# Performance work log

Measured on AMD Instinct MI355X. Metric: run time of the kernel, lower is better.

The kernel has to match this reference:

```python
import jax, jax.numpy as jnp
import numpy as np

B, T, D = 32, 2048, 128


def setup_inputs() -> dict:
    key = jax.random.key(0)
    k1, k2, k3 = jax.random.split(key, 3)
    values = jax.random.normal(k1, (B, T, D), dtype=jnp.float32)
    # monotonically increasing per-feature timestamps (irregular sampling)
    times = jnp.cumsum(jax.random.uniform(k2, (B, T, D), dtype=jnp.float32), axis=1)
    mask = jax.random.randint(k3, (B, T, D), 0, 2) > 0  # True = observed
    return {"values": values, "times": times, "mask": mask}


def _fill(x, t, mask):
    """Parallel forward fill (LOCF) and backward fill (NOCB) of x and t.

    Replaces the serial Keras RNN scan with cummax/cummin over observation
    indices followed by a gather. Matches ForwardCell semantics:
      forward : x init 0, t init times[:, 0, :]
      backward: x init 0, t init max(times, axis=1)
    """
    Tn = x.shape[1]
    ar = jnp.broadcast_to(jnp.arange(Tn, dtype=jnp.int32)[None, :, None], x.shape)
    # ---- forward fill ----
    fidx = jax.lax.cummax(jnp.where(mask, ar, -1), axis=1)  # last observed idx
    fvalid = fidx >= 0
    fi = jnp.clip(fidx, 0, Tn - 1)
    x_last = jnp.where(fvalid, jnp.take_along_axis(x, fi, axis=1), 0.0)
    t_last = jnp.where(fvalid, jnp.take_along_axis(t, fi, axis=1), t[:, :1, :])
    # ---- backward fill ----
    bidx = jax.lax.cummin(jnp.where(mask, ar, Tn), axis=1, reverse=True)  # next observed idx
    bvalid = bidx < Tn
    bi = jnp.clip(bidx, 0, Tn - 1)
    x_next = jnp.where(bvalid, jnp.take_along_axis(x, bi, axis=1), 0.0)
    t_next = jnp.where(bvalid, jnp.take_along_axis(t, bi, axis=1),
                       jnp.max(t, axis=1, keepdims=True))
    return x_last, t_last, x_next, t_next


def reference(values, times, mask):
    x_last, t_last, x_next, t_next = _fill(values, times, mask)
    denom = t_next - t_last
    num = x_last * (t_next - times) + x_next * (times - t_last)
    safe = denom != 0.0
    x_itp = num / jnp.where(safe, denom, 1.0)
    x_itp = jnp.where(safe & jnp.isfinite(x_itp), x_itp, 0.0)  # nan/inf -> 0
    return jnp.where(mask, values, x_itp)
```

## Files before the change

### kernel.cpp

```cpp
#include <hip/hip_runtime.h>
#include <math.h>

constexpr int B  = 32;
constexpr int T  = 2048;
constexpr int D  = 128;
constexpr int C  = 16;
constexpr int NC = T / C;

__global__ __launch_bounds__(256)
void linterp_kernel(const float* __restrict__ values,
                    const float* __restrict__ times,
                    const int*   __restrict__ mask,
                    float*       __restrict__ out)
{
    const int gid   = blockIdx.x * 256 + threadIdx.x;
    const int d     = gid & (D - 1);
    const int chunk = (gid >> 7) & (NC - 1);
    const int b     = gid >> 14;

    const int seq_base = b * T * D + d;
    const int t0i      = chunk * C;

    float v[C], tm[C];
    unsigned int mbits = 0;
#pragma unroll
    for (int i = 0; i < C; ++i) {
        const int off = seq_base + (t0i + i) * D;
        v[i]  = values[off];
        tm[i] = times[off];
        mbits |= (mask[off] != 0 ? 1u : 0u) << i;
    }

    const float t_first = times[seq_base];
    const float t_lastT = times[seq_base + (T - 1) * D];

    float fx = 0.f, ft = t_first;
    for (int j = t0i - 1; j >= 0; --j) {
        const int off = seq_base + j * D;
        if (mask[off] != 0) { fx = values[off]; ft = times[off]; break; }
    }

    float bx = 0.f, bt = t_lastT;
    for (int j = t0i + C; j < T; ++j) {
        const int off = seq_base + j * D;
        if (mask[off] != 0) { bx = values[off]; bt = times[off]; break; }
    }

    float xl[C], tl[C];
#pragma unroll
    for (int i = 0; i < C; ++i) {
        if ((mbits >> i) & 1u) { fx = v[i]; ft = tm[i]; }
        xl[i] = fx;
        tl[i] = ft;
    }

#pragma unroll
    for (int i = C - 1; i >= 0; --i) {
        const bool obs = (mbits >> i) & 1u;
        if (obs) { bx = v[i]; bt = tm[i]; }
        const float denom = bt - tl[i];
        const float num   = xl[i] * (bt - tm[i]) + bx * (tm[i] - tl[i]);
        const bool  safe  = (denom != 0.f);
        float xi = num / (safe ? denom : 1.f);
        xi = (safe && isfinite(xi)) ? xi : 0.f;
        out[seq_base + (t0i + i) * D] = obs ? v[i] : xi;
    }
}

extern "C" void kernel_launch(void* const* d_in, const int* in_sizes, int n_in,
                              void* d_out, int out_size, void* d_ws, size_t ws_size,
                              hipStream_t stream)
{
    const float* values = (const float*)d_in[0];
    const float* times  = (const float*)d_in[1];
    const int*   mask   = (const int*)d_in[2];
    float*       out    = (float*)d_out;

    const int total_threads = B * NC * D;
    linterp_kernel<<<total_threads / 256, 256, 0, stream>>>(values, times, mask, out);
}
```

Measured before the change: 143.0 us.

## Vectorize linear interpolation with float4 per thread and bitmap neighbor-chunk search

Each thread now handles four adjacent features via float4/int4 loads and stores, with the time chunk halved to 8 steps. The serial scalar search for the previous and next observation is replaced by one vectorized load of the neighboring chunk's mask, packed into bitmaps and resolved with clz/ctz. The scalar scan is kept as a fallback only when that neighbor chunk has no observation. This targets the many narrow, dependent loads and the low memory efficiency of the scalar version, at the cost of more registers per thread and fewer threads overall.

```diff
diff --git a/kernel.cpp b/kernel.cpp
--- a/kernel.cpp
+++ b/kernel.cpp
@@ -1,11 +1,12 @@
 #include <hip/hip_runtime.h>
 #include <math.h>
 
-constexpr int B  = 32;
-constexpr int T  = 2048;
-constexpr int D  = 128;
-constexpr int C  = 16;
-constexpr int NC = T / C;
+constexpr int B   = 32;
+constexpr int T   = 2048;
+constexpr int D   = 128;
+constexpr int C   = 8;
+constexpr int NCH = T / C;
+constexpr int DG  = D / 4;
 
 __global__ __launch_bounds__(256)
 void linterp_kernel(const float* __restrict__ values,
@@ -14,56 +15,117 @@
                     float*       __restrict__ out)
 {
     const int gid   = blockIdx.x * 256 + threadIdx.x;
-    const int d     = gid & (D - 1);
-    const int chunk = (gid >> 7) & (NC - 1);
-    const int b     = gid >> 14;
+    const int dg    = gid & (DG - 1);
+    const int chunk = (gid >> 5) & (NCH - 1);
+    const int b     = gid >> 13;
 
+    const int d        = dg * 4;
     const int seq_base = b * T * D + d;
     const int t0i      = chunk * C;
 
-    float v[C], tm[C];
-    unsigned int mbits = 0;
+    float4 xv[C], tmv[C], tlv[C];
+    unsigned int mb[4] = {0u, 0u, 0u, 0u};
 #pragma unroll
     for (int i = 0; i < C; ++i) {
         const int off = seq_base + (t0i + i) * D;
-        v[i]  = values[off];
-        tm[i] = times[off];
-        mbits |= (mask[off] != 0 ? 1u : 0u) << i;
+        xv[i]  = *(const float4*)(values + off);
+        tmv[i] = *(const float4*)(times + off);
+        const int4 m = *(const int4*)(mask + off);
+        mb[0] |= (m.x != 0 ? 1u : 0u) << i;
+        mb[1] |= (m.y != 0 ? 1u : 0u) << i;
+        mb[2] |= (m.z != 0 ? 1u : 0u) << i;
+        mb[3] |= (m.w != 0 ? 1u : 0u) << i;
     }
 
-    const float t_first = times[seq_base];
-    const float t_lastT = times[seq_base + (T - 1) * D];
+    const float4 t_first4 = *(const float4*)(times + seq_base);
+    const float4 t_lastT4 = *(const float4*)(times + seq_base + (T - 1) * D);
 
-    float fx = 0.f, ft = t_first;
-    for (int j = t0i - 1; j >= 0; --j) {
-        const int off = seq_base + j * D;
-        if (mask[off] != 0) { fx = values[off]; ft = times[off]; break; }
+    float fx[4] = {0.f, 0.f, 0.f, 0.f};
+    float ft[4] = {t_first4.x, t_first4.y, t_first4.z, t_first4.w};
+    if (chunk > 0) {
+        unsigned int pb[4] = {0u, 0u, 0u, 0u};
+#pragma unroll
+        for (int i = 0; i < C; ++i) {
+            const int4 m = *(const int4*)(mask + seq_base + (t0i - C + i) * D);
+            pb[0] |= (m.x != 0 ? 1u : 0u) << i;
+            pb[1] |= (m.y != 0 ? 1u : 0u) << i;
+            pb[2] |= (m.z != 0 ? 1u : 0u) << i;
+            pb[3] |= (m.w != 0 ? 1u : 0u) << i;
+        }
+#pragma unroll
+        for (int j = 0; j < 4; ++j) {
+            if (pb[j] != 0u) {
+                const int idx = 31 - __builtin_clz(pb[j]);
+                const int off = seq_base + (t0i - C + idx) * D + j;
+                fx[j] = values[off]; ft[j] = times[off];
+            } else {
+                for (int t = t0i - C - 1; t >= 0; --t) {
+                    const int off = seq_base + t * D + j;
+                    if (mask[off] != 0) { fx[j] = values[off]; ft[j] = times[off]; break; }
+                }
+            }
+        }
     }
 
-    float bx = 0.f, bt = t_lastT;
-    for (int j = t0i + C; j < T; ++j) {
-        const int off = seq_base + j * D;
-        if (mask[off] != 0) { bx = values[off]; bt = times[off]; break; }
+    float bx[4] = {0.f, 0.f, 0.f, 0.f};
+    float bt[4] = {t_lastT4.x, t_lastT4.y, t_lastT4.z, t_lastT4.w};
+    if (chunk < NCH - 1) {
+        unsigned int nb[4] = {0u, 0u, 0u, 0u};
+#pragma unroll
+        for (int i = 0; i < C; ++i) {
+            const int4 m = *(const int4*)(mask + seq_base + (t0i + C + i) * D);
+            nb[0] |= (m.x != 0 ? 1u : 0u) << i;
+            nb[1] |= (m.y != 0 ? 1u : 0u) << i;
+            nb[2] |= (m.z != 0 ? 1u : 0u) << i;
+            nb[3] |= (m.w != 0 ? 1u : 0u) << i;
+        }
+#pragma unroll
+        for (int j = 0; j < 4; ++j) {
+            if (nb[j] != 0u) {
+                const int idx = __builtin_ctz(nb[j]);
+                const int off = seq_base + (t0i + C + idx) * D + j;
+                bx[j] = values[off]; bt[j] = times[off];
+            } else {
+                for (int t = t0i + 2 * C; t < T; ++t) {
+                    const int off = seq_base + t * D + j;
+                    if (mask[off] != 0) { bx[j] = values[off]; bt[j] = times[off]; break; }
+                }
+            }
+        }
     }
 
-    float xl[C], tl[C];
 #pragma unroll
     for (int i = 0; i < C; ++i) {
-        if ((mbits >> i) & 1u) { fx = v[i]; ft = tm[i]; }
-        xl[i] = fx;
-        tl[i] = ft;
+        float* xp = (float*)&xv[i];
+        const float* tp = (const float*)&tmv[i];
+        float* lp = (float*)&tlv[i];
+#pragma unroll
+        for (int j = 0; j < 4; ++j) {
+            if ((mb[j] >> i) & 1u) { fx[j] = xp[j]; ft[j] = tp[j]; }
+            xp[j] = fx[j];
+            lp[j] = ft[j];
+        }
     }
 
 #pragma unroll
     for (int i = C - 1; i >= 0; --i) {
-        const bool obs = (mbits >> i) & 1u;
-        if (obs) { bx = v[i]; bt = tm[i]; }
-        const float denom = bt - tl[i];
-        const float num   = xl[i] * (bt - tm[i]) + bx * (tm[i] - tl[i]);
-        const bool  safe  = (denom != 0.f);
-        float xi = num / (safe ? denom : 1.f);
-        xi = (safe && isfinite(xi)) ? xi : 0.f;
-        out[seq_base + (t0i + i) * D] = obs ? v[i] : xi;
+        const float* xp = (const float*)&xv[i];
+        const float* tp = (const float*)&tmv[i];
+        const float* lp = (const float*)&tlv[i];
+        float4 o;
+        float* op = (float*)&o;
+#pragma unroll
+        for (int j = 0; j < 4; ++j) {
+            const bool obs = (mb[j] >> i) & 1u;
+            if (obs) { bx[j] = xp[j]; bt[j] = lp[j]; }
+            const float denom = bt[j] - lp[j];
+            const float num   = xp[j] * (bt[j] - tp[j]) + bx[j] * (tp[j] - lp[j]);
+            const bool  safe  = (denom != 0.f);
+            float xi = num / (safe ? denom : 1.f);
+            xi = (safe && isfinite(xi)) ? xi : 0.f;
+            op[j] = obs ? xp[j] : xi;
+        }
+        *(float4*)(out + seq_base + (t0i + i) * D) = o;
     }
 }
 
@@ -76,6 +138,6 @@
     const int*   mask   = (const int*)d_in[2];
     float*       out    = (float*)d_out;
 
-    const int total_threads = B * NC * D;
+    const int total_threads = B * NCH * DG;
     linterp_kernel<<<total_threads / 256, 256, 0, stream>>>(values, times, mask, out);
 }
```

Result: slower. 148.3 us (+3.7%).
